# Kernel optimization log

Measured on AMD Instinct MI355X. Metric: run time of the kernel, lower is better.

The kernel has to match this reference:

```python
import jax, jax.numpy as jnp
import numpy as np

H1 = 128
H2 = 128


def _lstm_cell(x, h, c, W_ih, W_hh, b_ih, b_hh):
    # x: [B, I], h/c: [B, H]; torch LSTMCell gate order: i, f, g, o
    gates = x @ W_ih.T + b_ih + h @ W_hh.T + b_hh  # [B, 4H]
    i, f, g, o = jnp.split(gates, 4, axis=-1)
    i = jax.nn.sigmoid(i)
    f = jax.nn.sigmoid(f)
    g = jnp.tanh(g)
    o = jax.nn.sigmoid(o)
    c_new = f * c + i * g
    h_new = o * jnp.tanh(c_new)
    return h_new, c_new


def setup_inputs() -> dict:
    key = jax.random.key(0)
    ks = jax.random.split(key, 12)
    B, T, I = 512, 1024, 1
    s1 = 1.0 / np.sqrt(H1)
    s2 = 1.0 / np.sqrt(H2)
    u = lambda k, shp, s: jax.random.uniform(k, shp, jnp.float32, -s, s)
    return {
        "input_seq": jax.random.normal(ks[0], (B, T), jnp.float32),
        "W_ih1": u(ks[1], (4 * H1, I), s1),
        "W_hh1": u(ks[2], (4 * H1, H1), s1),
        "b_ih1": u(ks[3], (4 * H1,), s1),
        "b_hh1": u(ks[4], (4 * H1,), s1),
        "W_ih2": u(ks[5], (4 * H2, H1), s2),
        "W_hh2": u(ks[6], (4 * H2, H2), s2),
        "b_ih2": u(ks[7], (4 * H2,), s2),
        "b_hh2": u(ks[8], (4 * H2,), s2),
        "W_out": u(ks[9], (1, H2), s2),
        "b_out": u(ks[10], (1,), s2),
    }


def reference(input_seq, W_ih1, W_hh1, b_ih1, b_hh1,
              W_ih2, W_hh2, b_ih2, b_hh2, W_out, b_out):
    B, T = input_seq.shape
    xs = input_seq.T[:, :, None]  # [T, B, 1]
    h1 = jnp.zeros((B, H1), input_seq.dtype)
    c1 = jnp.zeros((B, H1), input_seq.dtype)
    h2 = jnp.zeros((B, H2), input_seq.dtype)
    c2 = jnp.zeros((B, H2), input_seq.dtype)

    def step(carry, x_t):
        h1, c1, h2, c2 = carry
        h1, c1 = _lstm_cell(x_t, h1, c1, W_ih1, W_hh1, b_ih1, b_hh1)
        h2, c2 = _lstm_cell(h1, h2, c2, W_ih2, W_hh2, b_ih2, b_hh2)
        out_t = h2 @ W_out.T + b_out  # [B, 1]
        return (h1, c1, h2, c2), out_t[:, 0]

    _, outs = jax.lax.scan(step, (h1, c1, h2, c2), xs)  # outs: [T, B]
    return outs.T  # [B, T], matching torch.cat(outputs, dim=1)
```

## Files before the change

kernel.cpp:

```cpp
#include <hip/hip_runtime.h>

#define T_LEN 1024
#define HID   128
#define G4    512
#define NG    128
#define BCH   4
#define HB_STR 136

typedef _Float16 h2_t   __attribute__((ext_vector_type(2)));
typedef _Float16 f16x8  __attribute__((ext_vector_type(8)));
typedef float    f32x4n __attribute__((ext_vector_type(4)));

__device__ __forceinline__ float fsig(float v) {
  return __builtin_amdgcn_rcpf(1.0f + __expf(-v));
}
__device__ __forceinline__ float ftanh(float v) {
  float a = fabsf(v);
  float e = __expf(-2.0f * a);
  float t = (1.0f - e) * __builtin_amdgcn_rcpf(1.0f + e);
  return copysignf(t, v);
}

#define MFMA16(A, B, C) __builtin_amdgcn_mfma_f32_16x16x32_f16( \
    __builtin_bit_cast(f16x8, (A)), (B), (C), 0, 0, 0)

__global__ void __launch_bounds__(256) pack_frag2(
    const float* __restrict__ wa, const float* __restrict__ wb,
    const float* __restrict__ wc, uint4* __restrict__ dst) {
  int idx = blockIdx.x * 256 + threadIdx.x;
  int l = idx & 63;
  int f = (idx >> 6) & 15;
  int w = (idx >> 10) & 7;
  int m = idx >> 13;
  const float* src = (m == 0) ? wa : (m == 1) ? wb : wc;
  int row = (f >> 2) * HID + 16 * w + (l & 15);
  int k0  = 32 * (f & 3) + (l >> 4) * 8;
  const float* s = src + (size_t)row * HID + k0;
  unsigned int r[4];
#pragma unroll
  for (int qq = 0; qq < 4; ++qq) {
    h2_t h;
    h.x = (_Float16)s[2 * qq];
    h.y = (_Float16)s[2 * qq + 1];
    r[qq] = __builtin_bit_cast(unsigned int, h);
  }
  dst[idx] = make_uint4(r[0], r[1], r[2], r[3]);
}

__global__ void __launch_bounds__(512, 2) lstm_v14(
    const float* __restrict__ xin, const float* __restrict__ Wih1,
    const float* __restrict__ bih1, const float* __restrict__ bhh1,
    const uint4* __restrict__ wfrag,
    const float* __restrict__ bih2, const float* __restrict__ bhh2,
    const float* __restrict__ Wout, const float* __restrict__ bout,
    float* __restrict__ outp)
{
  __shared__ __align__(16) _Float16 hB1[2][2 * HB_STR];
  __shared__ __align__(16) _Float16 hB2[2][2 * HB_STR];
  __shared__ float prt[2][8][2];
  __shared__ float xbuf[2][T_LEN];
  __shared__ float outbuf[2][T_LEN];

  const int tid = threadIdx.x;
  const int l   = tid & 63;
  const int w   = tid >> 6;
  const int col = l & 15;
  const int q   = l >> 4;
  const int b0  = blockIdx.x * 2;

  const int b  = col & 1;
  const int s  = col >> 1;
  const int r_ = s & 3;
  const int Lc = s >> 2;
  const int u  = 16 * w + 4 * q + r_;

  f32x4n A1[16], A2[16], AI[16];
#pragma unroll
  for (int f = 0; f < 16; ++f) {
    A1[f] = __builtin_bit_cast(f32x4n, wfrag[((0 * 8 + w) * 16 + f) * 64 + l]);
    A2[f] = __builtin_bit_cast(f32x4n, wfrag[((1 * 8 + w) * 16 + f) * 64 + l]);
    AI[f] = __builtin_bit_cast(f32x4n, wfrag[((2 * 8 + w) * 16 + f) * 64 + l]);
  }
#pragma unroll
  for (int f = 0; f < 16; ++f)
    asm volatile("" : "+v"(A1[f]), "+v"(A2[f]), "+v"(AI[f]));

  float bc[4], wx[4];
#pragma unroll
  for (int g = 0; g < 4; ++g) {
    bc[g] = Lc ? (bih2[g * HID + u] + bhh2[g * HID + u])
               : (bih1[g * HID + u] + bhh1[g * HID + u]);
    wx[g] = Lc ? 0.f : Wih1[g * HID + u];
  }
  const float wo = Wout[u];
  const float bo = bout[0];
  float cst = 0.f;

#pragma unroll
  for (int i = 0; i < 4; ++i) {
    int idx = tid + 512 * i;
    int bq  = idx >> 10;
    int ps  = idx & 1023;
    xbuf[bq][ps] = xin[(size_t)(b0 + bq) * T_LEN + ps];
  }
  if (l < 2) { prt[0][w][l] = 0.f; prt[1][w][l] = 0.f; }
  __syncthreads();

  if (Lc == 0) {
    float xv = xbuf[b][0];
    float vi = fmaf(wx[0], xv, bc[0]);
    float vg = fmaf(wx[2], xv, bc[2]);
    float vo = fmaf(wx[3], xv, bc[3]);
    float si = fsig(vi), tg = ftanh(vg), so = fsig(vo);
    cst = si * tg;
    hB1[0][b * HB_STR + u] = (_Float16)(so * ftanh(cst));
  } else {
    hB2[0][b * HB_STR + u] = (_Float16)0.f;
  }
  __syncthreads();

  const int hb = b * HB_STR + q * 8;

  for (int t = 0; t < T_LEN; ++t) {
    const int p  = t & 1;
    const int pn = p ^ 1;

    f16x8 Bh0 = *reinterpret_cast<const f16x8*>(&hB1[p][hb +  0]);
    f16x8 Bh1 = *reinterpret_cast<const f16x8*>(&hB1[p][hb + 32]);
    f16x8 Bh2 = *reinterpret_cast<const f16x8*>(&hB1[p][hb + 64]);
    f16x8 Bh3 = *reinterpret_cast<const f16x8*>(&hB1[p][hb + 96]);
    f16x8 Dh0 = *reinterpret_cast<const f16x8*>(&hB2[p][hb +  0]);
    f16x8 Dh1 = *reinterpret_cast<const f16x8*>(&hB2[p][hb + 32]);
    f16x8 Dh2 = *reinterpret_cast<const f16x8*>(&hB2[p][hb + 64]);
    f16x8 Dh3 = *reinterpret_cast<const f16x8*>(&hB2[p][hb + 96]);

    f32x4n C1i = {0,0,0,0}, C1f = {0,0,0,0}, C1g = {0,0,0,0}, C1o = {0,0,0,0};
    f32x4n C2i = {0,0,0,0}, C2f = {0,0,0,0}, C2g = {0,0,0,0}, C2o = {0,0,0,0};

    C1i = MFMA16(A1[ 0], Bh0, C1i); C1i = MFMA16(A1[ 1], Bh1, C1i);
    C1i = MFMA16(A1[ 2], Bh2, C1i); C1i = MFMA16(A1[ 3], Bh3, C1i);
    C1f = MFMA16(A1[ 4], Bh0, C1f); C1f = MFMA16(A1[ 5], Bh1, C1f);
    C1f = MFMA16(A1[ 6], Bh2, C1f); C1f = MFMA16(A1[ 7], Bh3, C1f);
    C1g = MFMA16(A1[ 8], Bh0, C1g); C1g = MFMA16(A1[ 9], Bh1, C1g);
    C1g = MFMA16(A1[10], Bh2, C1g); C1g = MFMA16(A1[11], Bh3, C1g);
    C1o = MFMA16(A1[12], Bh0, C1o); C1o = MFMA16(A1[13], Bh1, C1o);
    C1o = MFMA16(A1[14], Bh2, C1o); C1o = MFMA16(A1[15], Bh3, C1o);

    C2i = MFMA16(A2[ 0], Dh0, C2i); C2i = MFMA16(A2[ 1], Dh1, C2i);
    C2i = MFMA16(A2[ 2], Dh2, C2i); C2i = MFMA16(A2[ 3], Dh3, C2i);
    C2f = MFMA16(A2[ 4], Dh0, C2f); C2f = MFMA16(A2[ 5], Dh1, C2f);
    C2f = MFMA16(A2[ 6], Dh2, C2f); C2f = MFMA16(A2[ 7], Dh3, C2f);
    C2g = MFMA16(A2[ 8], Dh0, C2g); C2g = MFMA16(A2[ 9], Dh1, C2g);
    C2g = MFMA16(A2[10], Dh2, C2g); C2g = MFMA16(A2[11], Dh3, C2g);
    C2o = MFMA16(A2[12], Dh0, C2o); C2o = MFMA16(A2[13], Dh1, C2o);
    C2o = MFMA16(A2[14], Dh2, C2o); C2o = MFMA16(A2[15], Dh3, C2o);

    C2i = MFMA16(AI[ 0], Bh0, C2i); C2i = MFMA16(AI[ 1], Bh1, C2i);
    C2i = MFMA16(AI[ 2], Bh2, C2i); C2i = MFMA16(AI[ 3], Bh3, C2i);
    C2f = MFMA16(AI[ 4], Bh0, C2f); C2f = MFMA16(AI[ 5], Bh1, C2f);
    C2f = MFMA16(AI[ 6], Bh2, C2f); C2f = MFMA16(AI[ 7], Bh3, C2f);
    C2g = MFMA16(AI[ 8], Bh0, C2g); C2g = MFMA16(AI[ 9], Bh1, C2g);
    C2g = MFMA16(AI[10], Bh2, C2g); C2g = MFMA16(AI[11], Bh3, C2g);
    C2o = MFMA16(AI[12], Bh0, C2o); C2o = MFMA16(AI[13], Bh1, C2o);
    C2o = MFMA16(AI[14], Bh2, C2o); C2o = MFMA16(AI[15], Bh3, C2o);

    if (tid < 2 && t > 0) {
      float sm = 0.f;
#pragma unroll
      for (int ww = 0; ww < 8; ++ww) sm += prt[p][ww][tid];
      outbuf[tid][t - 1] = sm;
    }

    {
      float Gi[4], Gf[4], Gg[4], Go[4];
#pragma unroll
      for (int j = 0; j < 4; ++j) {
        Gi[j] = Lc ? C2i[j] : C1i[j];
        Gf[j] = Lc ? C2f[j] : C1f[j];
        Gg[j] = Lc ? C2g[j] : C1g[j];
        Go[j] = Lc ? C2o[j] : C1o[j];
      }
      float vi = (r_ == 0) ? Gi[0] : (r_ == 1) ? Gi[1] : (r_ == 2) ? Gi[2] : Gi[3];
      float vf = (r_ == 0) ? Gf[0] : (r_ == 1) ? Gf[1] : (r_ == 2) ? Gf[2] : Gf[3];
      float vg = (r_ == 0) ? Gg[0] : (r_ == 1) ? Gg[1] : (r_ == 2) ? Gg[2] : Gg[3];
      float vo = (r_ == 0) ? Go[0] : (r_ == 1) ? Go[1] : (r_ == 2) ? Go[2] : Go[3];

      int tn = (t + 1) & (T_LEN - 1);
      float xv = xbuf[b][tn];
      vi += fmaf(wx[0], xv, bc[0]);
      vf += fmaf(wx[1], xv, bc[1]);
      vg += fmaf(wx[2], xv, bc[2]);
      vo += fmaf(wx[3], xv, bc[3]);
      float si = fsig(vi), sf = fsig(vf), tg = ftanh(vg), so = fsig(vo);
      cst = fmaf(sf, cst, si * tg);
      float hv = so * ftanh(cst);
      _Float16* hp = Lc ? &hB2[pn][0] : &hB1[pn][0];
      hp[b * HB_STR + u] = (_Float16)hv;

      float po = Lc ? wo * hv : 0.f;
      po += __shfl_xor(po,  2, 64);
      po += __shfl_xor(po,  4, 64);
      po += __shfl_xor(po,  8, 64);
      po += __shfl_xor(po, 16, 64);
      po += __shfl_xor(po, 32, 64);
      if (l < 2) prt[pn][w][l] = po;
    }
    __syncthreads();
  }

  if (tid < 2) {
    float sm = 0.f;
#pragma unroll
    for (int ww = 0; ww < 8; ++ww) sm += prt[0][ww][tid];
    outbuf[tid][T_LEN - 1] = sm;
  }
  __syncthreads();

#pragma unroll
  for (int i = 0; i < 4; ++i) {
    int idx = tid + 512 * i;
    int bq  = idx >> 10;
    int ps  = idx & 1023;
    outp[(size_t)(b0 + bq) * T_LEN + ps] = outbuf[bq][ps] + bo;
  }
}

__global__ void __launch_bounds__(512) transpose_w(
    const float* __restrict__ w1, const float* __restrict__ w2,
    const float* __restrict__ w3, float* __restrict__ o) {
  int m = blockIdx.y;
  const float* src = (m == 0) ? w1 : (m == 1) ? w2 : w3;
  float* dst = o + (size_t)m * G4 * HID;
  int idx = blockIdx.x * 512 + threadIdx.x;
  int j = idx >> 7;
  int k = idx & (HID - 1);
  dst[k * G4 + j] = src[idx];
}

__device__ __forceinline__ float gact(float v, int gt) {
  return (gt == 2) ? ftanh(v) : fsig(v);
}

__device__ __forceinline__ void store_out4(const float4* h2buf, float wo0, float wo1,
                                           float bo, int tid, int b0,
                                           float* __restrict__ outp, int t) {
  float4 ha = h2buf[tid];
  float4 hb = h2buf[tid + 64];
  float p0 = wo0 * ha.x + wo1 * hb.x;
  float p1 = wo0 * ha.y + wo1 * hb.y;
  float p2 = wo0 * ha.z + wo1 * hb.z;
  float p3 = wo0 * ha.w + wo1 * hb.w;
#pragma unroll
  for (int off = 1; off < 64; off <<= 1) {
    p0 += __shfl_xor(p0, off, 64);
    p1 += __shfl_xor(p1, off, 64);
    p2 += __shfl_xor(p2, off, 64);
    p3 += __shfl_xor(p3, off, 64);
  }
  if (tid < BCH) {
    float v = (tid == 0) ? p0 : (tid == 1) ? p1 : (tid == 2) ? p2 : p3;
    outp[(size_t)(b0 + tid) * T_LEN + t] = v + bo;
  }
}

__global__ void __launch_bounds__(512) lstm_fused(
    const float* __restrict__ xin, const float* __restrict__ Wih1,
    const float* __restrict__ bih1, const float* __restrict__ bhh1,
    const float* __restrict__ Whh1, const float* __restrict__ Wih2,
    const float* __restrict__ Whh2, int sk, int sj,
    const float* __restrict__ bih2, const float* __restrict__ bhh2,
    const float* __restrict__ Wout, const float* __restrict__ bout,
    float* __restrict__ outp) {
  __shared__ float4 h1buf[HID];
  __shared__ float4 h2buf[HID];
  __shared__ float4 g1[G4];
  __shared__ float4 g2[G4];
  __shared__ float xb[2][BCH];

  const int tid = threadIdx.x;
  const int b0 = blockIdx.x * BCH;
  const int gt = tid >> 7;

  float bias1 = bih1[tid] + bhh1[tid];
  float bias2 = bih2[tid] + bhh2[tid];
  float wi1 = Wih1[tid];
  float c1_0 = 0.f, c1_1 = 0.f, c1_2 = 0.f, c1_3 = 0.f;
  float c2_0 = 0.f, c2_1 = 0.f, c2_2 = 0.f, c2_3 = 0.f;
  float wo0 = 0.f, wo1 = 0.f, bo = 0.f;
  if (tid < 64) { wo0 = Wout[tid]; wo1 = Wout[tid + 64]; bo = bout[0]; }
  if (tid < HID) {
    h1buf[tid] = make_float4(0.f, 0.f, 0.f, 0.f);
    h2buf[tid] = make_float4(0.f, 0.f, 0.f, 0.f);
  }
  if (tid < BCH) xb[0][tid] = xin[(b0 + tid) * T_LEN];
  __syncthreads();

  const float* wp1  = Whh1 + tid * sj;
  const float* wp2  = Whh2 + tid * sj;
  const float* wpi2 = Wih2 + tid * sj;

  for (int t = 0; t < T_LEN; ++t) {
    float xpref = 0.f;
    if ((tid & ~3) == 128 && (t + 1) < T_LEN)
      xpref = xin[(b0 + (tid & 3)) * T_LEN + t + 1];

    if (tid < 64 && t > 0) store_out4(h2buf, wo0, wo1, bo, tid, b0, outp, t - 1);

    float xv0 = xb[t & 1][0], xv1 = xb[t & 1][1];
    float xv2 = xb[t & 1][2], xv3 = xb[t & 1][3];
    float a10 = fmaf(wi1, xv0, bias1);
    float a11 = fmaf(wi1, xv1, bias1);
    float a12 = fmaf(wi1, xv2, bias1);
    float a13 = fmaf(wi1, xv3, bias1);
    float a20 = bias2, a21 = bias2, a22 = bias2, a23 = bias2;
#pragma unroll 8
    for (int k = 0; k < HID; ++k) {
      float w1 = wp1[k * sk];
      float w2 = wp2[k * sk];
      float4 hv1 = h1buf[k];
      float4 hv2 = h2buf[k];
      a10 = fmaf(w1, hv1.x, a10);
      a11 = fmaf(w1, hv1.y, a11);
      a12 = fmaf(w1, hv1.z, a12);
      a13 = fmaf(w1, hv1.w, a13);
      a20 = fmaf(w2, hv2.x, a20);
      a21 = fmaf(w2, hv2.y, a21);
      a22 = fmaf(w2, hv2.z, a22);
      a23 = fmaf(w2, hv2.w, a23);
    }
    float4 A1v;
    A1v.x = gact(a10, gt); A1v.y = gact(a11, gt);
    A1v.z = gact(a12, gt); A1v.w = gact(a13, gt);
    g1[tid] = A1v;
    __syncthreads();

    if (tid < HID) {
      float4 iv = g1[tid], fv = g1[tid + HID];
      float4 gv = g1[tid + 2 * HID], ov = g1[tid + 3 * HID];
      c1_0 = fmaf(fv.x, c1_0, iv.x * gv.x);
      c1_1 = fmaf(fv.y, c1_1, iv.y * gv.y);
      c1_2 = fmaf(fv.z, c1_2, iv.z * gv.z);
      c1_3 = fmaf(fv.w, c1_3, iv.w * gv.w);
      float4 h;
      h.x = ov.x * ftanh(c1_0);
      h.y = ov.y * ftanh(c1_1);
      h.z = ov.z * ftanh(c1_2);
      h.w = ov.w * ftanh(c1_3);
      h1buf[tid] = h;
    }
    __syncthreads();

#pragma unroll 8
    for (int k = 0; k < HID; ++k) {
      float wv = wpi2[k * sk];
      float4 hv = h1buf[k];
      a20 = fmaf(wv, hv.x, a20);
      a21 = fmaf(wv, hv.y, a21);
      a22 = fmaf(wv, hv.z, a22);
      a23 = fmaf(wv, hv.w, a23);
    }
    float4 A2v;
    A2v.x = gact(a20, gt); A2v.y = gact(a21, gt);
    A2v.z = gact(a22, gt); A2v.w = gact(a23, gt);
    g2[tid] = A2v;
    __syncthreads();

    if (tid < HID) {
      float4 iv = g2[tid], fv = g2[tid + HID];
      float4 gv = g2[tid + 2 * HID], ov = g2[tid + 3 * HID];
      c2_0 = fmaf(fv.x, c2_0, iv.x * gv.x);
      c2_1 = fmaf(fv.y, c2_1, iv.y * gv.y);
      c2_2 = fmaf(fv.z, c2_2, iv.z * gv.z);
      c2_3 = fmaf(fv.w, c2_3, iv.w * gv.w);
      float4 h;
      h.x = ov.x * ftanh(c2_0);
      h.y = ov.y * ftanh(c2_1);
      h.z = ov.z * ftanh(c2_2);
      h.w = ov.w * ftanh(c2_3);
      h2buf[tid] = h;
    } else if ((tid & ~3) == 128 && (t + 1) < T_LEN) {
      xb[(t + 1) & 1][tid & 3] = xpref;
    }
    __syncthreads();
  }
  if (tid < 64) store_out4(h2buf, wo0, wo1, bo, tid, b0, outp, T_LEN - 1);
}

extern "C" void kernel_launch(void* const* d_in, const int* in_sizes, int n_in,
                              void* d_out, int out_size, void* d_ws, size_t ws_size,
                              hipStream_t stream) {
  const float* xin  = (const float*)d_in[0];
  const float* Wih1 = (const float*)d_in[1];
  const float* Whh1 = (const float*)d_in[2];
  const float* bih1 = (const float*)d_in[3];
  const float* bhh1 = (const float*)d_in[4];
  const float* Wih2 = (const float*)d_in[5];
  const float* Whh2 = (const float*)d_in[6];
  const float* bih2 = (const float*)d_in[7];
  const float* bhh2 = (const float*)d_in[8];
  const float* Wout = (const float*)d_in[9];
  const float* bout = (const float*)d_in[10];
  float* outp = (float*)d_out;

  const size_t needFr = (size_t)3 * 8 * 16 * 64 * sizeof(uint4);
  if (ws_size >= needFr) {
    uint4* wfrag = (uint4*)d_ws;
    pack_frag2<<<96, 256, 0, stream>>>(Whh1, Whh2, Wih2, wfrag);
    lstm_v14<<<256, 512, 0, stream>>>(
        xin, Wih1, bih1, bhh1, wfrag, bih2, bhh2, Wout, bout, outp);
    return;
  }

  size_t need = (size_t)3 * G4 * HID * sizeof(float);
  if (ws_size >= need) {
    float* wt = (float*)d_ws;
    transpose_w<<<dim3(128, 3), 512, 0, stream>>>(Whh1, Wih2, Whh2, wt);
    lstm_fused<<<NG, 512, 0, stream>>>(
        xin, Wih1, bih1, bhh1,
        wt, wt + (size_t)G4 * HID, wt + (size_t)2 * G4 * HID, G4, 1,
        bih2, bhh2, Wout, bout, outp);
  } else {
    lstm_fused<<<NG, 512, 0, stream>>>(
        xin, Wih1, bih1, bhh1,
        Whh1, Wih2, Whh2, 1, HID,
        bih2, bhh2, Wout, bout, outp);
  }
}
```

Measured before the change: 1.498 ms.

## Compute output projection from shared h2 via fdot2 in wave 0, unroll steps

The per-step output projection no longer goes through a cross-wave partial-sum array with full-wave shuffle reductions. Wave 0 now reads the previous h2 fragment it already loads for the MFMA B operand and forms the dot with Wout using packed fp16 fdot2 plus two shuffles. The time loop is unrolled by two so the ping-pong indices become compile-time constants. Layer-2 accumulation is split into separate chains for the recurrent and input terms to shorten dependent MFMA chains. In exchange, Wout and h2 are rounded to fp16 for the output dot, and wave 0 carries extra work and 16 more registers.

```diff
diff --git a/kernel.cpp b/kernel.cpp
--- a/kernel.cpp
+++ b/kernel.cpp
@@ -19,6 +19,11 @@
   float e = __expf(-2.0f * a);
   float t = (1.0f - e) * __builtin_amdgcn_rcpf(1.0f + e);
   return copysignf(t, v);
+}
+__device__ __forceinline__ float fdot2u(unsigned int a, unsigned int b, float c) {
+  union { unsigned int u; h2_t h; } ca, cb;
+  ca.u = a; cb.u = b;
+  return __builtin_amdgcn_fdot2(ca.h, cb.h, c, false);
 }
 
 #define MFMA16(A, B, C) __builtin_amdgcn_mfma_f32_16x16x32_f16( \
@@ -47,7 +52,7 @@
   dst[idx] = make_uint4(r[0], r[1], r[2], r[3]);
 }
 
-__global__ void __launch_bounds__(512, 2) lstm_v14(
+__global__ void __launch_bounds__(512, 2) lstm_v15(
     const float* __restrict__ xin, const float* __restrict__ Wih1,
     const float* __restrict__ bih1, const float* __restrict__ bhh1,
     const uint4* __restrict__ wfrag,
@@ -57,7 +62,6 @@
 {
   __shared__ __align__(16) _Float16 hB1[2][2 * HB_STR];
   __shared__ __align__(16) _Float16 hB2[2][2 * HB_STR];
-  __shared__ float prt[2][8][2];
   __shared__ float xbuf[2][T_LEN];
   __shared__ float outbuf[2][T_LEN];
 
@@ -92,9 +96,24 @@
                : (bih1[g * HID + u] + bhh1[g * HID + u]);
     wx[g] = Lc ? 0.f : Wih1[g * HID + u];
   }
-  const float wo = Wout[u];
   const float bo = bout[0];
   float cst = 0.f;
+
+  unsigned int woR[16];
+  if (w == 0) {
+#pragma unroll
+    for (int v = 0; v < 4; ++v)
+#pragma unroll
+      for (int jj = 0; jj < 4; ++jj) {
+        h2_t h;
+        h.x = (_Float16)Wout[32 * v + q * 8 + 2 * jj];
+        h.y = (_Float16)Wout[32 * v + q * 8 + 2 * jj + 1];
+        woR[4 * v + jj] = __builtin_bit_cast(unsigned int, h);
+      }
+  } else {
+#pragma unroll
+    for (int v = 0; v < 16; ++v) woR[v] = 0u;
+  }
 
 #pragma unroll
   for (int i = 0; i < 4; ++i) {
@@ -103,7 +122,6 @@
     int ps  = idx & 1023;
     xbuf[bq][ps] = xin[(size_t)(b0 + bq) * T_LEN + ps];
   }
-  if (l < 2) { prt[0][w][l] = 0.f; prt[1][w][l] = 0.f; }
   __syncthreads();
 
   if (Lc == 0) {
@@ -121,98 +139,116 @@
 
   const int hb = b * HB_STR + q * 8;
 
-  for (int t = 0; t < T_LEN; ++t) {
-    const int p  = t & 1;
-    const int pn = p ^ 1;
-
-    f16x8 Bh0 = *reinterpret_cast<const f16x8*>(&hB1[p][hb +  0]);
-    f16x8 Bh1 = *reinterpret_cast<const f16x8*>(&hB1[p][hb + 32]);
-    f16x8 Bh2 = *reinterpret_cast<const f16x8*>(&hB1[p][hb + 64]);
-    f16x8 Bh3 = *reinterpret_cast<const f16x8*>(&hB1[p][hb + 96]);
-    f16x8 Dh0 = *reinterpret_cast<const f16x8*>(&hB2[p][hb +  0]);
-    f16x8 Dh1 = *reinterpret_cast<const f16x8*>(&hB2[p][hb + 32]);
-    f16x8 Dh2 = *reinterpret_cast<const f16x8*>(&hB2[p][hb + 64]);
-    f16x8 Dh3 = *reinterpret_cast<const f16x8*>(&hB2[p][hb + 96]);
-
-    f32x4n C1i = {0,0,0,0}, C1f = {0,0,0,0}, C1g = {0,0,0,0}, C1o = {0,0,0,0};
-    f32x4n C2i = {0,0,0,0}, C2f = {0,0,0,0}, C2g = {0,0,0,0}, C2o = {0,0,0,0};
-
-    C1i = MFMA16(A1[ 0], Bh0, C1i); C1i = MFMA16(A1[ 1], Bh1, C1i);
-    C1i = MFMA16(A1[ 2], Bh2, C1i); C1i = MFMA16(A1[ 3], Bh3, C1i);
-    C1f = MFMA16(A1[ 4], Bh0, C1f); C1f = MFMA16(A1[ 5], Bh1, C1f);
-    C1f = MFMA16(A1[ 6], Bh2, C1f); C1f = MFMA16(A1[ 7], Bh3, C1f);
-    C1g = MFMA16(A1[ 8], Bh0, C1g); C1g = MFMA16(A1[ 9], Bh1, C1g);
-    C1g = MFMA16(A1[10], Bh2, C1g); C1g = MFMA16(A1[11], Bh3, C1g);
-    C1o = MFMA16(A1[12], Bh0, C1o); C1o = MFMA16(A1[13], Bh1, C1o);
-    C1o = MFMA16(A1[14], Bh2, C1o); C1o = MFMA16(A1[15], Bh3, C1o);
-
-    C2i = MFMA16(A2[ 0], Dh0, C2i); C2i = MFMA16(A2[ 1], Dh1, C2i);
-    C2i = MFMA16(A2[ 2], Dh2, C2i); C2i = MFMA16(A2[ 3], Dh3, C2i);
-    C2f = MFMA16(A2[ 4], Dh0, C2f); C2f = MFMA16(A2[ 5], Dh1, C2f);
-    C2f = MFMA16(A2[ 6], Dh2, C2f); C2f = MFMA16(A2[ 7], Dh3, C2f);
-    C2g = MFMA16(A2[ 8], Dh0, C2g); C2g = MFMA16(A2[ 9], Dh1, C2g);
-    C2g = MFMA16(A2[10], Dh2, C2g); C2g = MFMA16(A2[11], Dh3, C2g);
-    C2o = MFMA16(A2[12], Dh0, C2o); C2o = MFMA16(A2[13], Dh1, C2o);
-    C2o = MFMA16(A2[14], Dh2, C2o); C2o = MFMA16(A2[15], Dh3, C2o);
-
-    C2i = MFMA16(AI[ 0], Bh0, C2i); C2i = MFMA16(AI[ 1], Bh1, C2i);
-    C2i = MFMA16(AI[ 2], Bh2, C2i); C2i = MFMA16(AI[ 3], Bh3, C2i);
-    C2f = MFMA16(AI[ 4], Bh0, C2f); C2f = MFMA16(AI[ 5], Bh1, C2f);
-    C2f = MFMA16(AI[ 6], Bh2, C2f); C2f = MFMA16(AI[ 7], Bh3, C2f);
-    C2g = MFMA16(AI[ 8], Bh0, C2g); C2g = MFMA16(AI[ 9], Bh1, C2g);
-    C2g = MFMA16(AI[10], Bh2, C2g); C2g = MFMA16(AI[11], Bh3, C2g);
-    C2o = MFMA16(AI[12], Bh0, C2o); C2o = MFMA16(AI[13], Bh1, C2o);
-    C2o = MFMA16(AI[14], Bh2, C2o); C2o = MFMA16(AI[15], Bh3, C2o);
-
-    if (tid < 2 && t > 0) {
-      float sm = 0.f;
-#pragma unroll
-      for (int ww = 0; ww < 8; ++ww) sm += prt[p][ww][tid];
-      outbuf[tid][t - 1] = sm;
-    }
-
-    {
-      float Gi[4], Gf[4], Gg[4], Go[4];
-#pragma unroll
-      for (int j = 0; j < 4; ++j) {
-        Gi[j] = Lc ? C2i[j] : C1i[j];
-        Gf[j] = Lc ? C2f[j] : C1f[j];
-        Gg[j] = Lc ? C2g[j] : C1g[j];
-        Go[j] = Lc ? C2o[j] : C1o[j];
-      }
-      float vi = (r_ == 0) ? Gi[0] : (r_ == 1) ? Gi[1] : (r_ == 2) ? Gi[2] : Gi[3];
-      float vf = (r_ == 0) ? Gf[0] : (r_ == 1) ? Gf[1] : (r_ == 2) ? Gf[2] : Gf[3];
-      float vg = (r_ == 0) ? Gg[0] : (r_ == 1) ? Gg[1] : (r_ == 2) ? Gg[2] : Gg[3];
-      float vo = (r_ == 0) ? Go[0] : (r_ == 1) ? Go[1] : (r_ == 2) ? Go[2] : Go[3];
-
-      int tn = (t + 1) & (T_LEN - 1);
-      float xv = xbuf[b][tn];
-      vi += fmaf(wx[0], xv, bc[0]);
-      vf += fmaf(wx[1], xv, bc[1]);
-      vg += fmaf(wx[2], xv, bc[2]);
-      vo += fmaf(wx[3], xv, bc[3]);
-      float si = fsig(vi), sf = fsig(vf), tg = ftanh(vg), so = fsig(vo);
-      cst = fmaf(sf, cst, si * tg);
-      float hv = so * ftanh(cst);
-      _Float16* hp = Lc ? &hB2[pn][0] : &hB1[pn][0];
-      hp[b * HB_STR + u] = (_Float16)hv;
-
-      float po = Lc ? wo * hv : 0.f;
-      po += __shfl_xor(po,  2, 64);
-      po += __shfl_xor(po,  4, 64);
-      po += __shfl_xor(po,  8, 64);
-      po += __shfl_xor(po, 16, 64);
-      po += __shfl_xor(po, 32, 64);
-      if (l < 2) prt[pn][w][l] = po;
-    }
-    __syncthreads();
-  }
-
-  if (tid < 2) {
-    float sm = 0.f;
-#pragma unroll
-    for (int ww = 0; ww < 8; ++ww) sm += prt[0][ww][tid];
-    outbuf[tid][T_LEN - 1] = sm;
+#define LSTM_STEP(P, PN, TT)                                                  \
+  {                                                                           \
+    f16x8 Bh0 = *reinterpret_cast<const f16x8*>(&hB1[P][hb +  0]);            \
+    f16x8 Bh1 = *reinterpret_cast<const f16x8*>(&hB1[P][hb + 32]);            \
+    f16x8 Bh2 = *reinterpret_cast<const f16x8*>(&hB1[P][hb + 64]);            \
+    f16x8 Bh3 = *reinterpret_cast<const f16x8*>(&hB1[P][hb + 96]);            \
+    f16x8 Dh0 = *reinterpret_cast<const f16x8*>(&hB2[P][hb +  0]);            \
+    f16x8 Dh1 = *reinterpret_cast<const f16x8*>(&hB2[P][hb + 32]);            \
+    f16x8 Dh2 = *reinterpret_cast<const f16x8*>(&hB2[P][hb + 64]);            \
+    f16x8 Dh3 = *reinterpret_cast<const f16x8*>(&hB2[P][hb + 96]);            \
+    f32x4n C1i = {0,0,0,0}, C1f = {0,0,0,0}, C1g = {0,0,0,0}, C1o = {0,0,0,0};\
+    f32x4n Xi = {0,0,0,0}, Xf = {0,0,0,0}, Xg = {0,0,0,0}, Xo = {0,0,0,0};    \
+    f32x4n Yi = {0,0,0,0}, Yf = {0,0,0,0}, Yg = {0,0,0,0}, Yo = {0,0,0,0};    \
+    C1i = MFMA16(A1[ 0], Bh0, C1i); C1i = MFMA16(A1[ 1], Bh1, C1i);           \
+    C1i = MFMA16(A1[ 2], Bh2, C1i); C1i = MFMA16(A1[ 3], Bh3, C1i);           \
+    C1f = MFMA16(A1[ 4], Bh0, C1f); C1f = MFMA16(A1[ 5], Bh1, C1f);           \
+    C1f = MFMA16(A1[ 6], Bh2, C1f); C1f = MFMA16(A1[ 7], Bh3, C1f);           \
+    C1g = MFMA16(A1[ 8], Bh0, C1g); C1g = MFMA16(A1[ 9], Bh1, C1g);           \
+    C1g = MFMA16(A1[10], Bh2, C1g); C1g = MFMA16(A1[11], Bh3, C1g);           \
+    C1o = MFMA16(A1[12], Bh0, C1o); C1o = MFMA16(A1[13], Bh1, C1o);           \
+    C1o = MFMA16(A1[14], Bh2, C1o); C1o = MFMA16(A1[15], Bh3, C1o);           \
+    Xi = MFMA16(A2[ 0], Dh0, Xi); Xi = MFMA16(A2[ 1], Dh1, Xi);               \
+    Xi = MFMA16(A2[ 2], Dh2, Xi); Xi = MFMA16(A2[ 3], Dh3, Xi);               \
+    Xf = MFMA16(A2[ 4], Dh0, Xf); Xf = MFMA16(A2[ 5], Dh1, Xf);               \
+    Xf = MFMA16(A2[ 6], Dh2, Xf); Xf = MFMA16(A2[ 7], Dh3, Xf);               \
+    Xg = MFMA16(A2[ 8], Dh0, Xg); Xg = MFMA16(A2[ 9], Dh1, Xg);               \
+    Xg = MFMA16(A2[10], Dh2, Xg); Xg = MFMA16(A2[11], Dh3, Xg);               \
+    Xo = MFMA16(A2[12], Dh0, Xo); Xo = MFMA16(A2[13], Dh1, Xo);               \
+    Xo = MFMA16(A2[14], Dh2, Xo); Xo = MFMA16(A2[15], Dh3, Xo);               \
+    Yi = MFMA16(AI[ 0], Bh0, Yi); Yi = MFMA16(AI[ 1], Bh1, Yi);               \
+    Yi = MFMA16(AI[ 2], Bh2, Yi); Yi = MFMA16(AI[ 3], Bh3, Yi);               \
+    Yf = MFMA16(AI[ 4], Bh0, Yf); Yf = MFMA16(AI[ 5], Bh1, Yf);               \
+    Yf = MFMA16(AI[ 6], Bh2, Yf); Yf = MFMA16(AI[ 7], Bh3, Yf);               \
+    Yg = MFMA16(AI[ 8], Bh0, Yg); Yg = MFMA16(AI[ 9], Bh1, Yg);               \
+    Yg = MFMA16(AI[10], Bh2, Yg); Yg = MFMA16(AI[11], Bh3, Yg);               \
+    Yo = MFMA16(AI[12], Bh0, Yo); Yo = MFMA16(AI[13], Bh1, Yo);               \
+    Yo = MFMA16(AI[14], Bh2, Yo); Yo = MFMA16(AI[15], Bh3, Yo);               \
+    if (w == 0 && (TT) > 0) {                                                 \
+      uint4 d0 = __builtin_bit_cast(uint4, Dh0);                              \
+      uint4 d1 = __builtin_bit_cast(uint4, Dh1);                              \
+      uint4 d2 = __builtin_bit_cast(uint4, Dh2);                              \
+      uint4 d3 = __builtin_bit_cast(uint4, Dh3);                              \
+      float po = 0.f;                                                         \
+      po = fdot2u(woR[ 0], d0.x, po); po = fdot2u(woR[ 1], d0.y, po);         \
+      po = fdot2u(woR[ 2], d0.z, po); po = fdot2u(woR[ 3], d0.w, po);         \
+      po = fdot2u(woR[ 4], d1.x, po); po = fdot2u(woR[ 5], d1.y, po);         \
+      po = fdot2u(woR[ 6], d1.z, po); po = fdot2u(woR[ 7], d1.w, po);         \
+      po = fdot2u(woR[ 8], d2.x, po); po = fdot2u(woR[ 9], d2.y, po);         \
+      po = fdot2u(woR[10], d2.z, po); po = fdot2u(woR[11], d2.w, po);         \
+      po = fdot2u(woR[12], d3.x, po); po = fdot2u(woR[13], d3.y, po);         \
+      po = fdot2u(woR[14], d3.z, po); po = fdot2u(woR[15], d3.w, po);         \
+      po += __shfl_xor(po, 16, 64);                                           \
+      po += __shfl_xor(po, 32, 64);                                           \
+      if (l < 2) outbuf[l][(TT) - 1] = po;                                    \
+    }                                                                         \
+    {                                                                         \
+      float m_i[4], m_f[4], m_g[4], m_o[4];                                   \
+      _Pragma("unroll")                                                       \
+      for (int j = 0; j < 4; ++j) {                                           \
+        m_i[j] = Lc ? (Xi[j] + Yi[j]) : C1i[j];                               \
+        m_f[j] = Lc ? (Xf[j] + Yf[j]) : C1f[j];                               \
+        m_g[j] = Lc ? (Xg[j] + Yg[j]) : C1g[j];                               \
+        m_o[j] = Lc ? (Xo[j] + Yo[j]) : C1o[j];                               \
+      }                                                                       \
+      float vi = (r_ == 0) ? m_i[0] : (r_ == 1) ? m_i[1] : (r_ == 2) ? m_i[2] : m_i[3]; \
+      float vf = (r_ == 0) ? m_f[0] : (r_ == 1) ? m_f[1] : (r_ == 2) ? m_f[2] : m_f[3]; \
+      float vg = (r_ == 0) ? m_g[0] : (r_ == 1) ? m_g[1] : (r_ == 2) ? m_g[2] : m_g[3]; \
+      float vo = (r_ == 0) ? m_o[0] : (r_ == 1) ? m_o[1] : (r_ == 2) ? m_o[2] : m_o[3]; \
+      int tn = ((TT) + 1) & (T_LEN - 1);                                      \
+      float xv = xbuf[b][tn];                                                 \
+      vi += fmaf(wx[0], xv, bc[0]);                                           \
+      vf += fmaf(wx[1], xv, bc[1]);                                           \
+      vg += fmaf(wx[2], xv, bc[2]);                                           \
+      vo += fmaf(wx[3], xv, bc[3]);                                           \
+      float si = fsig(vi), sf = fsig(vf), tg = ftanh(vg), so = fsig(vo);      \
+      cst = fmaf(sf, cst, si * tg);                                           \
+      float hv = so * ftanh(cst);                                             \
+      _Float16* hp = Lc ? &hB2[PN][0] : &hB1[PN][0];                          \
+      hp[b * HB_STR + u] = (_Float16)hv;                                      \
+    }                                                                         \
+    __syncthreads();                                                          \
+  }
+
+  for (int t = 0; t < T_LEN; t += 2) {
+    LSTM_STEP(0, 1, t);
+    LSTM_STEP(1, 0, t + 1);
+  }
+#undef LSTM_STEP
+
+  if (w == 0) {
+    f16x8 Dh0 = *reinterpret_cast<const f16x8*>(&hB2[0][hb +  0]);
+    f16x8 Dh1 = *reinterpret_cast<const f16x8*>(&hB2[0][hb + 32]);
+    f16x8 Dh2 = *reinterpret_cast<const f16x8*>(&hB2[0][hb + 64]);
+    f16x8 Dh3 = *reinterpret_cast<const f16x8*>(&hB2[0][hb + 96]);
+    uint4 d0 = __builtin_bit_cast(uint4, Dh0);
+    uint4 d1 = __builtin_bit_cast(uint4, Dh1);
+    uint4 d2 = __builtin_bit_cast(uint4, Dh2);
+    uint4 d3 = __builtin_bit_cast(uint4, Dh3);
+    float po = 0.f;
+    po = fdot2u(woR[ 0], d0.x, po); po = fdot2u(woR[ 1], d0.y, po);
+    po = fdot2u(woR[ 2], d0.z, po); po = fdot2u(woR[ 3], d0.w, po);
+    po = fdot2u(woR[ 4], d1.x, po); po = fdot2u(woR[ 5], d1.y, po);
+    po = fdot2u(woR[ 6], d1.z, po); po = fdot2u(woR[ 7], d1.w, po);
+    po = fdot2u(woR[ 8], d2.x, po); po = fdot2u(woR[ 9], d2.y, po);
+    po = fdot2u(woR[10], d2.z, po); po = fdot2u(woR[11], d2.w, po);
+    po = fdot2u(woR[12], d3.x, po); po = fdot2u(woR[13], d3.y, po);
+    po = fdot2u(woR[14], d3.z, po); po = fdot2u(woR[15], d3.w, po);
+    po += __shfl_xor(po, 16, 64);
+    po += __shfl_xor(po, 32, 64);
+    if (l < 2) outbuf[l][T_LEN - 1] = po;
   }
   __syncthreads();
 
@@ -406,7 +442,7 @@
   if (ws_size >= needFr) {
     uint4* wfrag = (uint4*)d_ws;
     pack_frag2<<<96, 256, 0, stream>>>(Whh1, Whh2, Wih2, wfrag);
-    lstm_v14<<<256, 512, 0, stream>>>(
+    lstm_v15<<<256, 512, 0, stream>>>(
         xin, Wih1, bih1, bhh1, wfrag, bih2, bhh2, Wout, bout, outp);
     return;
   }
```

Result: slower. 3.526 ms (+135.3%).
